# Kernel optimization log

Measured on AMD Instinct MI355X. Metric: run time of the kernel, lower is better.

## Reference

```python
import jax, jax.numpy as jnp
import numpy as np

ORDER = 10


def setup_inputs() -> dict:
    key = jax.random.key(0)
    k1, k2, k3 = jax.random.split(key, 3)
    N, F, E = 100000, 128, 1600000
    x = jax.random.normal(k1, (N, F), dtype=jnp.float32)
    edge_index = jax.random.randint(k2, (2, E), 0, N, dtype=jnp.int64)
    # PPR initialization: w_k = alpha*(1-alpha)^k for k<order, w_order = (1-alpha)^order
    alpha = 0.1
    w = np.array([alpha * (1.0 - alpha) ** k for k in range(ORDER)] + [(1.0 - alpha) ** ORDER],
                 dtype=np.float32)
    weights = jnp.asarray(w)
    return {"x": x, "edge_index": edge_index, "weights": weights}


def _gcn_norm(edge_index, num_nodes):
    # add self loops
    loop = jnp.arange(num_nodes, dtype=edge_index.dtype)
    row = jnp.concatenate([edge_index[0], loop])  # source (x_j)
    col = jnp.concatenate([edge_index[1], loop])  # destination (aggregation)
    ones = jnp.ones(row.shape[0], dtype=jnp.float32)
    deg = jax.ops.segment_sum(ones, col, num_segments=num_nodes)
    deg_inv_sqrt = jnp.where(deg > 0, jax.lax.rsqrt(deg), 0.0)
    norm = deg_inv_sqrt[row] * deg_inv_sqrt[col]  # [E + N]
    return row, col, norm


def reference(x, edge_index, weights):
    N = x.shape[0]
    row, col, norm = _gcn_norm(edge_index, N)
    norm = norm.astype(x.dtype)[:, None]  # [E+N, 1]

    def propagate(h):
        # gather -> scale -> scatter-add  (symmetric normalized adjacency)
        return jax.ops.segment_sum(norm * h[row], col, num_segments=N)

    hidden = x
    out = weights[0] * hidden
    for k in range(1, ORDER + 1):
        hidden = propagate(hidden)
        out = out + weights[k] * hidden
    return out
```

## Files before the change

kernel.cpp:

```cpp
#include <hip/hip_runtime.h>
#include <hip/hip_fp16.h>


#define F 128
#define SCAN_B 256

__global__ void count_kernel(const int* __restrict__ ei, int E,
                             int* __restrict__ cnt) {
    int e = blockIdx.x * blockDim.x + threadIdx.x;
    if (e < E) {
        int c = ei[(size_t)E + e];
        atomicAdd(&cnt[c], 1);
    }
}

__global__ void dinv_kernel(const int* __restrict__ cnt, float* __restrict__ dinv,
                            int N) {
    int i = blockIdx.x * blockDim.x + threadIdx.x;
    if (i < N) {
        dinv[i] = rsqrtf((float)(cnt[i] + 1));
    }
}

__global__ void scan1_kernel(const int* __restrict__ cnt, int* __restrict__ offs,
                             int* __restrict__ bsums, int N) {
    __shared__ int sm[SCAN_B];
    int i = blockIdx.x * SCAN_B + threadIdx.x;
    int v = (i < N) ? cnt[i] : 0;
    sm[threadIdx.x] = v;
    __syncthreads();
    for (int d = 1; d < SCAN_B; d <<= 1) {
        int t = (threadIdx.x >= d) ? sm[threadIdx.x - d] : 0;
        __syncthreads();
        sm[threadIdx.x] += t;
        __syncthreads();
    }
    if (i < N) offs[i] = sm[threadIdx.x] - v;
    if (threadIdx.x == SCAN_B - 1) bsums[blockIdx.x] = sm[SCAN_B - 1];
}

__global__ void scan2_kernel(int* __restrict__ bsums, int nb) {
    __shared__ int sm[SCAN_B];
    __shared__ int carry;
    if (threadIdx.x == 0) carry = 0;
    __syncthreads();
    for (int base = 0; base < nb; base += SCAN_B) {
        int i = base + threadIdx.x;
        int v = (i < nb) ? bsums[i] : 0;
        sm[threadIdx.x] = v;
        __syncthreads();
        for (int d = 1; d < SCAN_B; d <<= 1) {
            int t = (threadIdx.x >= d) ? sm[threadIdx.x - d] : 0;
            __syncthreads();
            sm[threadIdx.x] += t;
            __syncthreads();
        }
        if (i < nb) bsums[i] = sm[threadIdx.x] - v + carry;
        __syncthreads();
        if (threadIdx.x == 0) carry += sm[SCAN_B - 1];
        __syncthreads();
    }
}

__global__ void scan3_kernel(int* __restrict__ offs, const int* __restrict__ bsums,
                             int* __restrict__ cursor, int N, int E) {
    int i = blockIdx.x * blockDim.x + threadIdx.x;
    if (i < N) {
        int o = offs[i] + bsums[i / SCAN_B];
        offs[i] = o;
        cursor[i] = o;
    }
    if (i == N) offs[N] = E;
}

__global__ void place_kernel(const int* __restrict__ ei, int E,
                             const float* __restrict__ dinv,
                             int* __restrict__ cursor, int2* __restrict__ edges) {
    int e = blockIdx.x * blockDim.x + threadIdx.x;
    if (e >= E) return;
    int r = ei[e];
    int c = ei[(size_t)E + e];
    int pos = atomicAdd(&cursor[c], 1);
    float w = dinv[r] * dinv[c];
    int2 p;
    p.x = r;
    p.y = __float_as_int(w);
    edges[pos] = p;
}

__global__ void conv_kernel(const float2* __restrict__ x2,
                            __half2* __restrict__ xh, __half2* __restrict__ y,
                            const float* __restrict__ wts, int order, int n2) {
    float wl = wts[order];
    for (int i = blockIdx.x * blockDim.x + threadIdx.x; i < n2;
         i += gridDim.x * blockDim.x) {
        float2 v = x2[i];
        xh[i] = __floats2half2_rn(v.x, v.y);
        y[i] = __floats2half2_rn(wl * v.x, wl * v.y);
    }
}

__global__ __launch_bounds__(128) void prop_kernel(
    const __half2* __restrict__ y_old, __half2* __restrict__ y_new,
    float2* __restrict__ out, const __half2* __restrict__ xh,
    const float* __restrict__ dinv, const int* __restrict__ offs,
    const int2* __restrict__ edges, const float* __restrict__ wts,
    int j, int last) {
    const int wave = threadIdx.x >> 6;
    const int lane = threadIdx.x & 63;
    const int c = (blockIdx.x << 1) + wave;
    const size_t rb = ((size_t)c << 6);

    const float wj = wts[j];
    const float dc = dinv[c];
    float2 hv = __half22float2(y_old[rb + lane]);
    float2 xv = __half22float2(xh[rb + lane]);
    const float s = dc * dc;
    float accx = fmaf(s, hv.x, wj * xv.x);
    float accy = fmaf(s, hv.y, wj * xv.y);

    int e = offs[c];
    const int end = offs[c + 1];

    for (; e + 8 <= end; e += 8) {
        int2 p0 = edges[e + 0];
        int2 p1 = edges[e + 1];
        int2 p2 = edges[e + 2];
        int2 p3 = edges[e + 3];
        int2 p4 = edges[e + 4];
        int2 p5 = edges[e + 5];
        int2 p6 = edges[e + 6];
        int2 p7 = edges[e + 7];
        float2 f0 = __half22float2(y_old[((size_t)p0.x << 6) + lane]);
        float2 f1 = __half22float2(y_old[((size_t)p1.x << 6) + lane]);
        float2 f2 = __half22float2(y_old[((size_t)p2.x << 6) + lane]);
        float2 f3 = __half22float2(y_old[((size_t)p3.x << 6) + lane]);
        float2 f4 = __half22float2(y_old[((size_t)p4.x << 6) + lane]);
        float2 f5 = __half22float2(y_old[((size_t)p5.x << 6) + lane]);
        float2 f6 = __half22float2(y_old[((size_t)p6.x << 6) + lane]);
        float2 f7 = __half22float2(y_old[((size_t)p7.x << 6) + lane]);
        accx = fmaf(__int_as_float(p0.y), f0.x, accx);
        accy = fmaf(__int_as_float(p0.y), f0.y, accy);
        accx = fmaf(__int_as_float(p1.y), f1.x, accx);
        accy = fmaf(__int_as_float(p1.y), f1.y, accy);
        accx = fmaf(__int_as_float(p2.y), f2.x, accx);
        accy = fmaf(__int_as_float(p2.y), f2.y, accy);
        accx = fmaf(__int_as_float(p3.y), f3.x, accx);
        accy = fmaf(__int_as_float(p3.y), f3.y, accy);
        accx = fmaf(__int_as_float(p4.y), f4.x, accx);
        accy = fmaf(__int_as_float(p4.y), f4.y, accy);
        accx = fmaf(__int_as_float(p5.y), f5.x, accx);
        accy = fmaf(__int_as_float(p5.y), f5.y, accy);
        accx = fmaf(__int_as_float(p6.y), f6.x, accx);
        accy = fmaf(__int_as_float(p6.y), f6.y, accy);
        accx = fmaf(__int_as_float(p7.y), f7.x, accx);
        accy = fmaf(__int_as_float(p7.y), f7.y, accy);
    }
    for (; e < end; ++e) {
        int2 p = edges[e];
        float2 f = __half22float2(y_old[((size_t)p.x << 6) + lane]);
        accx = fmaf(__int_as_float(p.y), f.x, accx);
        accy = fmaf(__int_as_float(p.y), f.y, accy);
    }

    if (last) {
        float2 o;
        o.x = accx;
        o.y = accy;
        out[rb + lane] = o;
    } else {
        y_new[rb + lane] = __floats2half2_rn(accx, accy);
    }
}

extern "C" void kernel_launch(void* const* d_in, const int* in_sizes, int n_in,
                              void* d_out, int out_size, void* d_ws, size_t ws_size,
                              hipStream_t stream) {
    const float* x = (const float*)d_in[0];
    const int* ei = (const int*)d_in[1];
    const float* wts = (const float*)d_in[2];
    float2* out = (float2*)d_out;

    const int NF = in_sizes[0];
    const int N = NF / F;
    const int E = in_sizes[1] / 2;
    const int order = in_sizes[2] - 1;

    char* p = (char*)d_ws;
    auto carve = [&](size_t bytes) {
        void* q = (void*)p;
        p += (bytes + 255) & ~(size_t)255;
        return q;
    };
    int nb = (N + SCAN_B - 1) / SCAN_B;
    int*     cnt   = (int*)carve(sizeof(int) * (size_t)N);
    int*     offs  = (int*)carve(sizeof(int) * (size_t)(N + 1));
    int*     bsums = (int*)carve(sizeof(int) * (size_t)nb);
    float*   dinv  = (float*)carve(sizeof(float) * (size_t)N);
    int2*    edges = (int2*)carve(8ull * (size_t)E);
    __half2* xh    = (__half2*)carve(sizeof(__half2) * (size_t)(NF / 2));
    __half2* yA    = (__half2*)carve(sizeof(__half2) * (size_t)(NF / 2));
    __half2* yB    = (__half2*)carve(sizeof(__half2) * (size_t)(NF / 2));
    int*     cursor = cnt;
    (void)ws_size;

    hipMemsetAsync(cnt, 0, sizeof(int) * (size_t)N, stream);
    count_kernel<<<(E + 255) / 256, 256, 0, stream>>>(ei, E, cnt);
    dinv_kernel<<<(N + 255) / 256, 256, 0, stream>>>(cnt, dinv, N);
    scan1_kernel<<<nb, SCAN_B, 0, stream>>>(cnt, offs, bsums, N);
    scan2_kernel<<<1, SCAN_B, 0, stream>>>(bsums, nb);
    scan3_kernel<<<(N + 1 + 255) / 256, 256, 0, stream>>>(offs, bsums, cursor, N, E);
    place_kernel<<<(E + 255) / 256, 256, 0, stream>>>(ei, E, dinv, cursor, edges);

    conv_kernel<<<2048, 256, 0, stream>>>((const float2*)x, xh, yA, wts, order,
                                          NF / 2);

    const __half2* yin = yA;
    __half2* yout = yB;
    for (int j = order - 1; j >= 0; --j) {
        int last = (j == 0);
        prop_kernel<<<N / 2, 128, 0, stream>>>(yin, yout, out, xh, dinv, offs,
                                               edges, wts, j, last);
        yin = yout;
        yout = (yout == yA) ? yB : yA;
    }
}
```

Before: 927.4 us.

## Store CSR edges as source indices only and partition placement by destination range

The CSR edge array now holds only the 4-byte source index, and each propagation step recomputes the edge weight from the dinv table, halving edge-array traffic in every step. The placement kernel is restructured into 8 groups, each scanning all edges but only placing those whose destination falls in its node range, which localizes the cursor atomics and scattered writes. The cost is an extra random dinv gather per edge in the propagation kernel and 8x reads of the edge list during setup.

```diff
diff --git a/kernel.cpp b/kernel.cpp
--- a/kernel.cpp
+++ b/kernel.cpp
@@ -4,6 +4,7 @@
 
 #define F 128
 #define SCAN_B 256
+#define NGROUP 8
 
 __global__ void count_kernel(const int* __restrict__ ei, int E,
                              int* __restrict__ cnt) {
@@ -74,18 +75,20 @@
 }
 
 __global__ void place_kernel(const int* __restrict__ ei, int E,
-                             const float* __restrict__ dinv,
-                             int* __restrict__ cursor, int2* __restrict__ edges) {
-    int e = blockIdx.x * blockDim.x + threadIdx.x;
-    if (e >= E) return;
-    int r = ei[e];
-    int c = ei[(size_t)E + e];
-    int pos = atomicAdd(&cursor[c], 1);
-    float w = dinv[r] * dinv[c];
-    int2 p;
-    p.x = r;
-    p.y = __float_as_int(w);
-    edges[pos] = p;
+                             int* __restrict__ cursor, int* __restrict__ edges,
+                             int N) {
+    const int g = blockIdx.x & (NGROUP - 1);
+    const int b = blockIdx.x >> 3;
+    const int nb = gridDim.x >> 3;
+    const int lo = (int)((long long)N * g / NGROUP);
+    const int hi = (int)((long long)N * (g + 1) / NGROUP);
+    const int stride = nb * blockDim.x;
+    for (int e = b * blockDim.x + threadIdx.x; e < E; e += stride) {
+        int c = ei[(size_t)E + e];
+        if (c < lo || c >= hi) continue;
+        int pos = atomicAdd(&cursor[c], 1);
+        edges[pos] = ei[e];
+    }
 }
 
 __global__ void conv_kernel(const float2* __restrict__ x2,
@@ -104,7 +107,7 @@
     const __half2* __restrict__ y_old, __half2* __restrict__ y_new,
     float2* __restrict__ out, const __half2* __restrict__ xh,
     const float* __restrict__ dinv, const int* __restrict__ offs,
-    const int2* __restrict__ edges, const float* __restrict__ wts,
+    const int* __restrict__ edges, const float* __restrict__ wts,
     int j, int last) {
     const int wave = threadIdx.x >> 6;
     const int lane = threadIdx.x & 63;
@@ -123,44 +126,53 @@
     const int end = offs[c + 1];
 
     for (; e + 8 <= end; e += 8) {
-        int2 p0 = edges[e + 0];
-        int2 p1 = edges[e + 1];
-        int2 p2 = edges[e + 2];
-        int2 p3 = edges[e + 3];
-        int2 p4 = edges[e + 4];
-        int2 p5 = edges[e + 5];
-        int2 p6 = edges[e + 6];
-        int2 p7 = edges[e + 7];
-        float2 f0 = __half22float2(y_old[((size_t)p0.x << 6) + lane]);
-        float2 f1 = __half22float2(y_old[((size_t)p1.x << 6) + lane]);
-        float2 f2 = __half22float2(y_old[((size_t)p2.x << 6) + lane]);
-        float2 f3 = __half22float2(y_old[((size_t)p3.x << 6) + lane]);
-        float2 f4 = __half22float2(y_old[((size_t)p4.x << 6) + lane]);
-        float2 f5 = __half22float2(y_old[((size_t)p5.x << 6) + lane]);
-        float2 f6 = __half22float2(y_old[((size_t)p6.x << 6) + lane]);
-        float2 f7 = __half22float2(y_old[((size_t)p7.x << 6) + lane]);
-        accx = fmaf(__int_as_float(p0.y), f0.x, accx);
-        accy = fmaf(__int_as_float(p0.y), f0.y, accy);
-        accx = fmaf(__int_as_float(p1.y), f1.x, accx);
-        accy = fmaf(__int_as_float(p1.y), f1.y, accy);
-        accx = fmaf(__int_as_float(p2.y), f2.x, accx);
-        accy = fmaf(__int_as_float(p2.y), f2.y, accy);
-        accx = fmaf(__int_as_float(p3.y), f3.x, accx);
-        accy = fmaf(__int_as_float(p3.y), f3.y, accy);
-        accx = fmaf(__int_as_float(p4.y), f4.x, accx);
-        accy = fmaf(__int_as_float(p4.y), f4.y, accy);
-        accx = fmaf(__int_as_float(p5.y), f5.x, accx);
-        accy = fmaf(__int_as_float(p5.y), f5.y, accy);
-        accx = fmaf(__int_as_float(p6.y), f6.x, accx);
-        accy = fmaf(__int_as_float(p6.y), f6.y, accy);
-        accx = fmaf(__int_as_float(p7.y), f7.x, accx);
-        accy = fmaf(__int_as_float(p7.y), f7.y, accy);
+        int s0 = edges[e + 0];
+        int s1 = edges[e + 1];
+        int s2 = edges[e + 2];
+        int s3 = edges[e + 3];
+        int s4 = edges[e + 4];
+        int s5 = edges[e + 5];
+        int s6 = edges[e + 6];
+        int s7 = edges[e + 7];
+        float w0 = dinv[s0] * dc;
+        float w1 = dinv[s1] * dc;
+        float w2 = dinv[s2] * dc;
+        float w3 = dinv[s3] * dc;
+        float w4 = dinv[s4] * dc;
+        float w5 = dinv[s5] * dc;
+        float w6 = dinv[s6] * dc;
+        float w7 = dinv[s7] * dc;
+        float2 f0 = __half22float2(y_old[((size_t)s0 << 6) + lane]);
+        float2 f1 = __half22float2(y_old[((size_t)s1 << 6) + lane]);
+        float2 f2 = __half22float2(y_old[((size_t)s2 << 6) + lane]);
+        float2 f3 = __half22float2(y_old[((size_t)s3 << 6) + lane]);
+        float2 f4 = __half22float2(y_old[((size_t)s4 << 6) + lane]);
+        float2 f5 = __half22float2(y_old[((size_t)s5 << 6) + lane]);
+        float2 f6 = __half22float2(y_old[((size_t)s6 << 6) + lane]);
+        float2 f7 = __half22float2(y_old[((size_t)s7 << 6) + lane]);
+        accx = fmaf(w0, f0.x, accx);
+        accy = fmaf(w0, f0.y, accy);
+        accx = fmaf(w1, f1.x, accx);
+        accy = fmaf(w1, f1.y, accy);
+        accx = fmaf(w2, f2.x, accx);
+        accy = fmaf(w2, f2.y, accy);
+        accx = fmaf(w3, f3.x, accx);
+        accy = fmaf(w3, f3.y, accy);
+        accx = fmaf(w4, f4.x, accx);
+        accy = fmaf(w4, f4.y, accy);
+        accx = fmaf(w5, f5.x, accx);
+        accy = fmaf(w5, f5.y, accy);
+        accx = fmaf(w6, f6.x, accx);
+        accy = fmaf(w6, f6.y, accy);
+        accx = fmaf(w7, f7.x, accx);
+        accy = fmaf(w7, f7.y, accy);
     }
     for (; e < end; ++e) {
-        int2 p = edges[e];
-        float2 f = __half22float2(y_old[((size_t)p.x << 6) + lane]);
-        accx = fmaf(__int_as_float(p.y), f.x, accx);
-        accy = fmaf(__int_as_float(p.y), f.y, accy);
+        int s0 = edges[e];
+        float w0 = dinv[s0] * dc;
+        float2 f = __half22float2(y_old[((size_t)s0 << 6) + lane]);
+        accx = fmaf(w0, f.x, accx);
+        accy = fmaf(w0, f.y, accy);
     }
 
     if (last) {
@@ -197,7 +209,7 @@
     int*     offs  = (int*)carve(sizeof(int) * (size_t)(N + 1));
     int*     bsums = (int*)carve(sizeof(int) * (size_t)nb);
     float*   dinv  = (float*)carve(sizeof(float) * (size_t)N);
-    int2*    edges = (int2*)carve(8ull * (size_t)E);
+    int*     edges = (int*)carve(4ull * (size_t)E);
     __half2* xh    = (__half2*)carve(sizeof(__half2) * (size_t)(NF / 2));
     __half2* yA    = (__half2*)carve(sizeof(__half2) * (size_t)(NF / 2));
     __half2* yB    = (__half2*)carve(sizeof(__half2) * (size_t)(NF / 2));
@@ -210,7 +222,7 @@
     scan1_kernel<<<nb, SCAN_B, 0, stream>>>(cnt, offs, bsums, N);
     scan2_kernel<<<1, SCAN_B, 0, stream>>>(bsums, nb);
     scan3_kernel<<<(N + 1 + 255) / 256, 256, 0, stream>>>(offs, bsums, cursor, N, E);
-    place_kernel<<<(E + 255) / 256, 256, 0, stream>>>(ei, E, dinv, cursor, edges);
+    place_kernel<<<2048, 256, 0, stream>>>(ei, E, cursor, edges, N);
 
     conv_kernel<<<2048, 256, 0, stream>>>((const float2*)x, xh, yA, wts, order,
                                           NF / 2);
```

New measurement: 913.2 us. Within noise of the previous version (-1.5%).
